# Kernel tuning notes

Hardware: AMD Instinct MI355X
Metric: run time of the kernel (lower is better)

## Reference

```python
import jax, jax.numpy as jnp
import numpy as np
import math

N = 12288
IN_MAIN, IN_MOD = 64, 128
NC_INNER, NC_QK, OUT_MAIN = 16, 8, 64

def setup_inputs() -> dict:
    key = jax.random.key(0)
    ks = jax.random.split(key, 8)
    s = lambda fan_in: 1.0 / np.sqrt(fan_in)
    return {
        "x_main": jax.random.normal(ks[0], (N, IN_MAIN), dtype=jnp.float32),
        "x_mod": jax.random.normal(ks[1], (N, IN_MOD), dtype=jnp.float32),
        "xyz": jax.random.uniform(ks[2], (N, 3), dtype=jnp.float32),
        # MLP E: [in_main+in_mod -> nc_inner -> nc_inner], bias=False (weights stored [in, out])
        "W_e1": jax.random.uniform(ks[3], (IN_MAIN + IN_MOD, NC_INNER), jnp.float32, -s(IN_MAIN + IN_MOD), s(IN_MAIN + IN_MOD)),
        "W_e2": jax.random.uniform(ks[4], (NC_INNER, NC_INNER), jnp.float32, -s(NC_INNER), s(NC_INNER)),
        "W_q": jax.random.uniform(ks[5], (NC_INNER, NC_QK), jnp.float32, -s(NC_INNER), s(NC_INNER)),
        "W_k": jax.random.uniform(ks[6], (NC_INNER, NC_QK), jnp.float32, -s(NC_INNER), s(NC_INNER)),
        "W_v": jax.random.uniform(ks[7], (NC_INNER, OUT_MAIN), jnp.float32, -s(NC_INNER), s(NC_INNER)),
    }

def reference(x_main, x_mod, xyz, W_e1, W_e2, W_q, W_k, W_v):
    # concat 3D + 2D features: [N, in_main+in_mod]
    x = jnp.concatenate((x_main, x_mod), axis=-1)
    # MLP E (bias-free Linear + ReLU per layer): [N, nc_inner]
    h = jax.nn.relu(jax.nn.relu(x @ W_e1) @ W_e2)
    Q = h @ W_q  # [N, nc_qk]
    K = h @ W_k  # [N, nc_qk]
    V = h @ W_v  # [N, out_main]
    scale = 1.0 / math.sqrt(NC_QK)
    scores = (Q @ K.T) * scale          # [N, N] full global attention
    attn = jax.nn.softmax(scores, axis=1)
    return attn @ V                     # [N, out_main]
```

## Files before the change

kernel.cpp:

```cpp
#include <hip/hip_runtime.h>
#include <stdint.h>


#define NN 12288

typedef float    f32x16 __attribute__((ext_vector_type(16)));
typedef short    s16x8  __attribute__((ext_vector_type(8)));
typedef unsigned short u16;

#define MFMA_32x32x16_BF16 __builtin_amdgcn_mfma_f32_32x32x16_bf16

#define OFF_QB   0u
#define OFF_KB   196608u
#define OFF_VT   393216u
#define OFF_PO   2162688u

typedef __attribute__((address_space(3))) void lds_void_t;
typedef const __attribute__((address_space(1))) void gbl_void_t;
__device__ __forceinline__ void gld16(const void* g, void* l) {
    __builtin_amdgcn_global_load_lds((gbl_void_t*)g, (lds_void_t*)l, 16, 0, 0);
}

__device__ __forceinline__ float bf2f(u16 s) {
    union { unsigned int u; float f; } c; c.u = ((unsigned int)s) << 16; return c.f;
}
__device__ __forceinline__ u16 f2bf(float f) {
    union { float f; unsigned int u; } c; c.f = f;
    return (u16)((c.u + 0x8000u) >> 16);
}
__device__ __forceinline__ unsigned int pk2(float a, float b) {
    union { float f; unsigned int u; } ca, cb; ca.f = a; cb.f = b;
    return ((ca.u + 0x8000u) >> 16) | ((cb.u + 0x8000u) & 0xffff0000u);
}
__device__ __forceinline__ f32x16 zf16() {
    f32x16 z;
#pragma unroll
    for (int i = 0; i < 16; ++i) z[i] = 0.f;
    return z;
}
__device__ __forceinline__ s16x8 zs8() {
    s16x8 z;
#pragma unroll
    for (int i = 0; i < 8; ++i) z[i] = 0;
    return z;
}

union U8 { s16x8 v; unsigned int u[4]; };

__global__ __launch_bounds__(256) void k1_qkv(
    const void* __restrict__ xmain, const void* __restrict__ xmod,
    const void* __restrict__ we1, const void* __restrict__ we2,
    const void* __restrict__ wqp, const void* __restrict__ wkp,
    const void* __restrict__ wvp,
    u16* __restrict__ qb, u16* __restrict__ kb, u16* __restrict__ vt)
{
    __shared__ float wf[4608];
    __shared__ int   sflag;
    __shared__ float lh1[64][4][17];
    __shared__ float lh2[64][17];

    const int t = threadIdx.x;
    const int r = t >> 2;
    const int p = t & 3;
    const int row = blockIdx.x * 64 + r;

    if (t == 0) sflag = 0;
    __syncthreads();
    {
        float v = bf2f(((const u16*)xmod)[2 * t]);
        if (fabsf(v) > 16.f) atomicAdd(&sflag, 1);
    }
    __syncthreads();
    const int isf32 = (sflag > 8);

    const float SCL = 0.51006979f;
    if (isf32) {
        const float* a1 = (const float*)we1; const float* a2 = (const float*)we2;
        const float* aq = (const float*)wqp; const float* ak = (const float*)wkp;
        const float* av = (const float*)wvp;
        for (int i = t; i < 4608; i += 256) {
            if      (i < 3072) wf[i] = a1[i];
            else if (i < 3328) wf[i] = a2[i - 3072];
            else if (i < 3456) wf[i] = aq[i - 3328] * SCL;
            else if (i < 3584) wf[i] = ak[i - 3456];
            else               wf[i] = av[i - 3584];
        }
    } else {
        const u16* a1 = (const u16*)we1; const u16* a2 = (const u16*)we2;
        const u16* aq = (const u16*)wqp; const u16* ak = (const u16*)wkp;
        const u16* av = (const u16*)wvp;
        for (int i = t; i < 4608; i += 256) {
            if      (i < 3072) wf[i] = bf2f(a1[i]);
            else if (i < 3328) wf[i] = bf2f(a2[i - 3072]);
            else if (i < 3456) wf[i] = bf2f(aq[i - 3328]) * SCL;
            else if (i < 3584) wf[i] = bf2f(ak[i - 3456]);
            else               wf[i] = bf2f(av[i - 3584]);
        }
    }
    __syncthreads();

    const float* __restrict__ W1 = wf;
    const float* __restrict__ W2 = wf + 3072;
    const float* __restrict__ Wq = wf + 3328;
    const float* __restrict__ Wk = wf + 3456;
    const float* __restrict__ Wv = wf + 3584;

    float h1p[16];
#pragma unroll
    for (int o = 0; o < 16; ++o) h1p[o] = 0.f;

    if (isf32) {
#pragma unroll
        for (int cc = 0; cc < 12; ++cc) {
            const int c = p + cc * 4;
            float4 xv = (c < 16)
                ? ((const float4*)xmain)[(size_t)row * 16 + c]
                : ((const float4*)xmod)[(size_t)row * 32 + (c - 16)];
            float xs[4] = {xv.x, xv.y, xv.z, xv.w};
#pragma unroll
            for (int j = 0; j < 4; ++j) {
                const float* wr = W1 + (c * 4 + j) * 16;
#pragma unroll
                for (int o = 0; o < 16; ++o) h1p[o] += xs[j] * wr[o];
            }
        }
    } else {
#pragma unroll
        for (int cc = 0; cc < 12; ++cc) {
            const int c = p + cc * 4;
            uint2 xv = (c < 16)
                ? ((const uint2*)xmain)[(size_t)row * 16 + c]
                : ((const uint2*)xmod)[(size_t)row * 32 + (c - 16)];
            float xs[4] = { bf2f((u16)(xv.x & 0xffff)), bf2f((u16)(xv.x >> 16)),
                            bf2f((u16)(xv.y & 0xffff)), bf2f((u16)(xv.y >> 16)) };
#pragma unroll
            for (int j = 0; j < 4; ++j) {
                const float* wr = W1 + (c * 4 + j) * 16;
#pragma unroll
                for (int o = 0; o < 16; ++o) h1p[o] += xs[j] * wr[o];
            }
        }
    }
#pragma unroll
    for (int o = 0; o < 16; ++o) lh1[r][p][o] = h1p[o];
    __syncthreads();

    float h1[16];
#pragma unroll
    for (int o = 0; o < 16; ++o)
        h1[o] = fmaxf(lh1[r][0][o] + lh1[r][1][o] + lh1[r][2][o] + lh1[r][3][o], 0.f);

#pragma unroll
    for (int oo = 0; oo < 4; ++oo) {
        const int o = p * 4 + oo;
        float s = 0.f;
#pragma unroll
        for (int j = 0; j < 16; ++j) s += h1[j] * W2[j * 16 + o];
        lh2[r][o] = fmaxf(s, 0.f);
    }
    __syncthreads();

    float h2[16];
#pragma unroll
    for (int j = 0; j < 16; ++j) h2[j] = lh2[r][j];

    {
        float q0 = 0.f, q1 = 0.f, k0 = 0.f, k1 = 0.f;
        const int o = 2 * p;
#pragma unroll
        for (int j = 0; j < 16; ++j) {
            q0 += h2[j] * Wq[j * 8 + o];
            q1 += h2[j] * Wq[j * 8 + o + 1];
            k0 += h2[j] * Wk[j * 8 + o];
            k1 += h2[j] * Wk[j * 8 + o + 1];
        }
        ((unsigned int*)qb)[(size_t)row * 4 + p] = pk2(q0, q1);
        ((unsigned int*)kb)[(size_t)row * 4 + p] = pk2(k0, k1);
    }

    const int tI = row >> 5, kk = row & 31;
#pragma unroll
    for (int c16 = 0; c16 < 16; ++c16) {
        const int c = p * 16 + c16;
        float v = 0.f;
#pragma unroll
        for (int j = 0; j < 16; ++j) v += h2[j] * Wv[j * 64 + c];
        vt[(size_t)tI * 2304 + c * 36 + kk] = f2bf(v);
    }
}

__global__ __launch_bounds__(256, 4) void k2_attn(
    const u16* __restrict__ qb, const u16* __restrict__ kb,
    const u16* __restrict__ vt,
    float* __restrict__ po, float* __restrict__ pl,
    int nsplit, int tiles)
{
    __shared__ union SM {
        uint4 stage[4][2][288];
        struct { float lo[4][64][33]; float ll[4][32]; } ep;
    } sm;

    const int tid  = threadIdx.x;
    const int lane = tid & 63;
    const int half = lane >> 5;
    const int l31  = lane & 31;
    const int w    = tid >> 6;
    const int qt   = blockIdx.x % 384;
    const int sp   = blockIdx.x / 384;
    const int qbase = qt * 32;
    const int key_start = sp * (NN / nsplit) + w * (tiles * 32);
    const int t0 = key_start >> 5;

    const f32x16 Z = zf16();
    s16x8 qf = zs8();
    if (!half) qf = *(const s16x8*)(qb + (size_t)(qbase + l31) * 8);

    f32x16 acc0 = Z, acc1 = Z;
    float ls = 0.f;

    {
        const char* g = (const char*)vt + (size_t)t0 * 4608 + lane * 16;
#pragma unroll
        for (int j = 0; j < 4; ++j)
            gld16(g + j * 1024, &sm.stage[w][0][j * 64]);
        if (lane < 32)
            gld16(g + 4096, &sm.stage[w][0][256]);
    }
    s16x8 ka_c = *(const s16x8*)(kb + (size_t)(key_start + l31) * 8);

    for (int kt = 0; kt < tiles; ++kt) {
        __builtin_amdgcn_s_waitcnt(0x0F70);
        const int cb = kt & 1;
        const bool has_next = (kt + 1 < tiles);

        s16x8 ka_n;
        if (has_next) {
            ka_n = *(const s16x8*)(kb + (size_t)(key_start + (kt + 1) * 32 + l31) * 8);
            const char* g = (const char*)vt + (size_t)(t0 + kt + 1) * 4608 + lane * 16;
#pragma unroll
            for (int j = 0; j < 4; ++j)
                gld16(g + j * 1024, &sm.stage[w][cb ^ 1][j * 64]);
            if (lane < 32)
                gld16(g + 4096, &sm.stage[w][cb ^ 1][256]);
        }

        f32x16 S = MFMA_32x32x16_BF16(ka_c, qf, Z, 0, 0, 0);

        float pr[16];
        float ls0 = 0.f, ls1 = 0.f;
#pragma unroll
        for (int r = 0; r < 8; ++r) {
            pr[r]     = __builtin_amdgcn_exp2f(S[r]);
            pr[r + 8] = __builtin_amdgcn_exp2f(S[r + 8]);
            ls0 += pr[r];
            ls1 += pr[r + 8];
        }
        ls += ls0 + ls1;

        U8 pb0, pb1;
#pragma unroll
        for (int i = 0; i < 4; ++i) {
            pb0.u[i] = pk2(pr[2 * i],     pr[2 * i + 1]);
            pb1.u[i] = pk2(pr[8 + 2 * i], pr[8 + 2 * i + 1]);
        }

        const u16* base = (const u16*)&sm.stage[w][cb][0];
        const u16* r0 = base + l31 * 36 + 4 * half;
        const u16* r1 = base + (32 + l31) * 36 + 4 * half;
        U8 va;
        uint2 x0, x1;
        x0 = *(const uint2*)(r0);       x1 = *(const uint2*)(r0 + 8);
        va.u[0] = x0.x; va.u[1] = x0.y; va.u[2] = x1.x; va.u[3] = x1.y;
        acc0 = MFMA_32x32x16_BF16(va.v, pb0.v, acc0, 0, 0, 0);
        x0 = *(const uint2*)(r1);       x1 = *(const uint2*)(r1 + 8);
        va.u[0] = x0.x; va.u[1] = x0.y; va.u[2] = x1.x; va.u[3] = x1.y;
        acc1 = MFMA_32x32x16_BF16(va.v, pb0.v, acc1, 0, 0, 0);
        x0 = *(const uint2*)(r0 + 16);  x1 = *(const uint2*)(r0 + 24);
        va.u[0] = x0.x; va.u[1] = x0.y; va.u[2] = x1.x; va.u[3] = x1.y;
        acc0 = MFMA_32x32x16_BF16(va.v, pb1.v, acc0, 0, 0, 0);
        x0 = *(const uint2*)(r1 + 16);  x1 = *(const uint2*)(r1 + 24);
        va.u[0] = x0.x; va.u[1] = x0.y; va.u[2] = x1.x; va.u[3] = x1.y;
        acc1 = MFMA_32x32x16_BF16(va.v, pb1.v, acc1, 0, 0, 0);

        if (has_next) ka_c = ka_n;
    }

    __syncthreads();

    ls += __shfl_xor(ls, 32, 64);
    if (lane < 32) sm.ep.ll[w][l31] = ls;
#pragma unroll
    for (int r = 0; r < 16; ++r) {
        const int c = (r & 3) + 8 * (r >> 2) + 4 * half;
        sm.ep.lo[w][c][l31]      = acc0[r];
        sm.ep.lo[w][32 + c][l31] = acc1[r];
    }
    __syncthreads();

    const int rq = tid >> 3;
    const int c0 = (tid & 7) * 8;
    float o[8];
#pragma unroll
    for (int j = 0; j < 8; ++j) {
        o[j] = sm.ep.lo[0][c0 + j][rq] + sm.ep.lo[1][c0 + j][rq] +
               sm.ep.lo[2][c0 + j][rq] + sm.ep.lo[3][c0 + j][rq];
    }
    float4* pov = (float4*)(po + (size_t)sp * (NN * 64) +
                            (size_t)(qbase + rq) * 64 + c0);
    pov[0] = make_float4(o[0], o[1], o[2], o[3]);
    pov[1] = make_float4(o[4], o[5], o[6], o[7]);
    if (tid < 32)
        pl[(size_t)sp * NN + qbase + tid] =
            sm.ep.ll[0][tid] + sm.ep.ll[1][tid] + sm.ep.ll[2][tid] + sm.ep.ll[3][tid];
}

__global__ __launch_bounds__(256) void k3_norm(
    const float4* __restrict__ po, const float* __restrict__ pl,
    float4* __restrict__ out, int nsplit)
{
    const int i = blockIdx.x * 256 + threadIdx.x;
    const int row = i >> 4;
    float l = 0.f;
    float4 o = make_float4(0.f, 0.f, 0.f, 0.f);
    for (int s = 0; s < nsplit; ++s) {
        l += pl[(size_t)s * NN + row];
        float4 p = po[(size_t)s * (NN * 16) + i];
        o.x += p.x; o.y += p.y; o.z += p.z; o.w += p.w;
    }
    const float rl = 1.0f / l;
    out[i] = make_float4(o.x * rl, o.y * rl, o.z * rl, o.w * rl);
}

extern "C" void kernel_launch(void* const* d_in, const int* in_sizes, int n_in,
                              void* d_out, int out_size, void* d_ws, size_t ws_size,
                              hipStream_t stream)
{
    const void* xmain = d_in[0];
    const void* xmod  = d_in[1];
    const void* we1   = d_in[3];
    const void* we2   = d_in[4];
    const void* wq    = d_in[5];
    const void* wk    = d_in[6];
    const void* wv    = d_in[7];

    char* ws = (char*)d_ws;
    u16*   qb   = (u16*)  (ws + OFF_QB);
    u16*   kb   = (u16*)  (ws + OFF_KB);
    u16*   vt   = (u16*)  (ws + OFF_VT);

    int S = 1;
    for (int cand = 8; cand >= 1; cand >>= 1) {
        size_t need = (size_t)OFF_PO + (size_t)cand * (NN * 64 * 4) +
                      (size_t)cand * (NN * 4);
        if (ws_size >= need) { S = cand; break; }
    }
    float* po = (float*)(ws + OFF_PO);
    float* pl = po + (size_t)S * (NN * 64);
    const int tiles = NN / (128 * S);

    k1_qkv<<<192, 256, 0, stream>>>(xmain, xmod, we1, we2, wq, wk, wv,
                                    qb, kb, vt);
    k2_attn<<<384 * S, 256, 0, stream>>>(qb, kb, vt, po, pl, S, tiles);
    k3_norm<<<768, 256, 0, stream>>>((const float4*)po, pl, (float4*)d_out, S);
}
```

Before: 131.2 us.

## Share V tiles across four query waves and store bf16 split partials

The attention kernel is restructured so each block's four waves handle four different 32-row query tiles over the same key range. They cooperatively load one shared double-buffered V tile instead of each wave streaming its own key slice, which cuts LDS use and global V traffic per query and allows higher occupancy (launch bound 4 to 6) and up to 16 key splits. Partial outputs are stored as bf16 instead of fp32 to halve partial-sum traffic, and a hardware packed bf16 conversion builtin is used when available. The cost is a block-wide barrier on every key tile and extra rounding error in the split partials.

New measurement: 131.2 us. About the same (-0.0%).

```diff
diff --git a/kernel.cpp b/kernel.cpp
--- a/kernel.cpp
+++ b/kernel.cpp
@@ -31,6 +31,14 @@
 __device__ __forceinline__ unsigned int pk2(float a, float b) {
     union { float f; unsigned int u; } ca, cb; ca.f = a; cb.f = b;
     return ((ca.u + 0x8000u) >> 16) | ((cb.u + 0x8000u) & 0xffff0000u);
+}
+__device__ __forceinline__ unsigned int pkbf(float a, float b) {
+#if __has_builtin(__builtin_amdgcn_cvt_pk_bf16_f32)
+    auto r = __builtin_amdgcn_cvt_pk_bf16_f32(a, b);
+    union { decltype(r) v; unsigned int u; } c; c.v = r; return c.u;
+#else
+    return pk2(a, b);
+#endif
 }
 __device__ __forceinline__ f32x16 zf16() {
     f32x16 z;
@@ -189,15 +197,15 @@
     }
 }
 
-__global__ __launch_bounds__(256, 4) void k2_attn(
+__global__ __launch_bounds__(256, 6) void k2_attn(
     const u16* __restrict__ qb, const u16* __restrict__ kb,
     const u16* __restrict__ vt,
-    float* __restrict__ po, float* __restrict__ pl,
+    u16* __restrict__ po, float* __restrict__ pl,
     int nsplit, int tiles)
 {
     __shared__ union SM {
-        uint4 stage[4][2][288];
-        struct { float lo[4][64][33]; float ll[4][32]; } ep;
+        uint4 stage[2][288];
+        float sf[2304];
     } sm;
 
     const int tid  = threadIdx.x;
@@ -205,43 +213,41 @@
     const int half = lane >> 5;
     const int l31  = lane & 31;
     const int w    = tid >> 6;
-    const int qt   = blockIdx.x % 384;
-    const int sp   = blockIdx.x / 384;
-    const int qbase = qt * 32;
-    const int key_start = sp * (NN / nsplit) + w * (tiles * 32);
+    const int qB   = (blockIdx.x % 96) * 128;
+    const int sp   = blockIdx.x / 96;
+    const int myq  = qB + 32 * w;
+    const int key_start = sp * (NN / nsplit);
     const int t0 = key_start >> 5;
 
     const f32x16 Z = zf16();
     s16x8 qf = zs8();
-    if (!half) qf = *(const s16x8*)(qb + (size_t)(qbase + l31) * 8);
+    if (!half) qf = *(const s16x8*)(qb + (size_t)(myq + l31) * 8);
 
     f32x16 acc0 = Z, acc1 = Z;
     float ls = 0.f;
 
     {
-        const char* g = (const char*)vt + (size_t)t0 * 4608 + lane * 16;
-#pragma unroll
-        for (int j = 0; j < 4; ++j)
-            gld16(g + j * 1024, &sm.stage[w][0][j * 64]);
-        if (lane < 32)
-            gld16(g + 4096, &sm.stage[w][0][256]);
+        const char* g = (const char*)vt + (size_t)t0 * 4608 + 1152 * w + lane * 16;
+        char* l = (char*)&sm.stage[0][0] + 1152 * w;
+        gld16(g, l);
+        if (lane < 8) gld16(g + 1024, l + 1024);
     }
     s16x8 ka_c = *(const s16x8*)(kb + (size_t)(key_start + l31) * 8);
 
     for (int kt = 0; kt < tiles; ++kt) {
         __builtin_amdgcn_s_waitcnt(0x0F70);
+        __syncthreads();
         const int cb = kt & 1;
         const bool has_next = (kt + 1 < tiles);
 
         s16x8 ka_n;
         if (has_next) {
             ka_n = *(const s16x8*)(kb + (size_t)(key_start + (kt + 1) * 32 + l31) * 8);
-            const char* g = (const char*)vt + (size_t)(t0 + kt + 1) * 4608 + lane * 16;
-#pragma unroll
-            for (int j = 0; j < 4; ++j)
-                gld16(g + j * 1024, &sm.stage[w][cb ^ 1][j * 64]);
-            if (lane < 32)
-                gld16(g + 4096, &sm.stage[w][cb ^ 1][256]);
+            const char* g = (const char*)vt + (size_t)(t0 + kt + 1) * 4608
+                          + 1152 * w + lane * 16;
+            char* l = (char*)&sm.stage[cb ^ 1][0] + 1152 * w;
+            gld16(g, l);
+            if (lane < 8) gld16(g + 1024, l + 1024);
         }
 
         f32x16 S = MFMA_32x32x16_BF16(ka_c, qf, Z, 0, 0, 0);
@@ -260,11 +266,11 @@
         U8 pb0, pb1;
 #pragma unroll
         for (int i = 0; i < 4; ++i) {
-            pb0.u[i] = pk2(pr[2 * i],     pr[2 * i + 1]);
-            pb1.u[i] = pk2(pr[8 + 2 * i], pr[8 + 2 * i + 1]);
-        }
-
-        const u16* base = (const u16*)&sm.stage[w][cb][0];
+            pb0.u[i] = pkbf(pr[2 * i],     pr[2 * i + 1]);
+            pb1.u[i] = pkbf(pr[8 + 2 * i], pr[8 + 2 * i + 1]);
+        }
+
+        const u16* base = (const u16*)&sm.stage[cb][0];
         const u16* r0 = base + l31 * 36 + 4 * half;
         const u16* r1 = base + (32 + l31) * 36 + 4 * half;
         U8 va;
@@ -285,50 +291,52 @@
         if (has_next) ka_c = ka_n;
     }
 
-    __syncthreads();
-
     ls += __shfl_xor(ls, 32, 64);
-    if (lane < 32) sm.ep.ll[w][l31] = ls;
-#pragma unroll
-    for (int r = 0; r < 16; ++r) {
-        const int c = (r & 3) + 8 * (r >> 2) + 4 * half;
-        sm.ep.lo[w][c][l31]      = acc0[r];
-        sm.ep.lo[w][32 + c][l31] = acc1[r];
-    }
-    __syncthreads();
-
-    const int rq = tid >> 3;
-    const int c0 = (tid & 7) * 8;
-    float o[8];
-#pragma unroll
-    for (int j = 0; j < 8; ++j) {
-        o[j] = sm.ep.lo[0][c0 + j][rq] + sm.ep.lo[1][c0 + j][rq] +
-               sm.ep.lo[2][c0 + j][rq] + sm.ep.lo[3][c0 + j][rq];
-    }
-    float4* pov = (float4*)(po + (size_t)sp * (NN * 64) +
-                            (size_t)(qbase + rq) * 64 + c0);
-    pov[0] = make_float4(o[0], o[1], o[2], o[3]);
-    pov[1] = make_float4(o[4], o[5], o[6], o[7]);
-    if (tid < 32)
-        pl[(size_t)sp * NN + qbase + tid] =
-            sm.ep.ll[0][tid] + sm.ep.ll[1][tid] + sm.ep.ll[2][tid] + sm.ep.ll[3][tid];
+
+    u16* poS = po + (size_t)sp * (NN * 64);
+    for (int j = 0; j < 4; ++j) {
+        __syncthreads();
+        if (w == j) {
+#pragma unroll
+            for (int r = 0; r < 16; ++r) {
+                const int c = (r & 3) + 8 * (r >> 2) + 4 * half;
+                sm.sf[c * 33 + l31]        = acc0[r];
+                sm.sf[(32 + c) * 33 + l31] = acc1[r];
+            }
+            if (lane < 32) sm.sf[2112 + l31] = ls;
+        }
+        __syncthreads();
+        const int rq = tid >> 3;
+        const int c0 = (tid & 7) * 8;
+        unsigned int u0 = pkbf(sm.sf[(c0 + 0) * 33 + rq], sm.sf[(c0 + 1) * 33 + rq]);
+        unsigned int u1 = pkbf(sm.sf[(c0 + 2) * 33 + rq], sm.sf[(c0 + 3) * 33 + rq]);
+        unsigned int u2 = pkbf(sm.sf[(c0 + 4) * 33 + rq], sm.sf[(c0 + 5) * 33 + rq]);
+        unsigned int u3 = pkbf(sm.sf[(c0 + 6) * 33 + rq], sm.sf[(c0 + 7) * 33 + rq]);
+        *(uint4*)(poS + (size_t)(qB + 32 * j + rq) * 64 + c0) =
+            make_uint4(u0, u1, u2, u3);
+        if (tid < 32)
+            pl[(size_t)sp * NN + qB + 32 * j + tid] = sm.sf[2112 + tid];
+    }
 }
 
 __global__ __launch_bounds__(256) void k3_norm(
-    const float4* __restrict__ po, const float* __restrict__ pl,
+    const u16* __restrict__ po, const float* __restrict__ pl,
     float4* __restrict__ out, int nsplit)
 {
     const int i = blockIdx.x * 256 + threadIdx.x;
     const int row = i >> 4;
+    const int c0 = (i & 15) * 4;
     float l = 0.f;
-    float4 o = make_float4(0.f, 0.f, 0.f, 0.f);
+    float o0 = 0.f, o1 = 0.f, o2 = 0.f, o3 = 0.f;
     for (int s = 0; s < nsplit; ++s) {
         l += pl[(size_t)s * NN + row];
-        float4 p = po[(size_t)s * (NN * 16) + i];
-        o.x += p.x; o.y += p.y; o.z += p.z; o.w += p.w;
+        uint2 p = *(const uint2*)(po + (size_t)s * (NN * 64) +
+                                  (size_t)row * 64 + c0);
+        o0 += bf2f((u16)(p.x & 0xffff)); o1 += bf2f((u16)(p.x >> 16));
+        o2 += bf2f((u16)(p.y & 0xffff)); o3 += bf2f((u16)(p.y >> 16));
     }
     const float rl = 1.0f / l;
-    out[i] = make_float4(o.x * rl, o.y * rl, o.z * rl, o.w * rl);
+    out[i] = make_float4(o0 * rl, o1 * rl, o2 * rl, o3 * rl);
 }
 
 extern "C" void kernel_launch(void* const* d_in, const int* in_sizes, int n_in,
@@ -349,17 +357,17 @@
     u16*   vt   = (u16*)  (ws + OFF_VT);
 
     int S = 1;
-    for (int cand = 8; cand >= 1; cand >>= 1) {
-        size_t need = (size_t)OFF_PO + (size_t)cand * (NN * 64 * 4) +
+    for (int cand = 16; cand >= 1; cand >>= 1) {
+        size_t need = (size_t)OFF_PO + (size_t)cand * (NN * 64 * 2) +
                       (size_t)cand * (NN * 4);
         if (ws_size >= need) { S = cand; break; }
     }
-    float* po = (float*)(ws + OFF_PO);
-    float* pl = po + (size_t)S * (NN * 64);
-    const int tiles = NN / (128 * S);
+    u16*   po = (u16*)(ws + OFF_PO);
+    float* pl = (float*)(ws + OFF_PO + (size_t)S * (NN * 64 * 2));
+    const int tiles = NN / (32 * S);
 
     k1_qkv<<<192, 256, 0, stream>>>(xmain, xmod, we1, we2, wq, wk, wv,
                                     qb, kb, vt);
-    k2_attn<<<384 * S, 256, 0, stream>>>(qb, kb, vt, po, pl, S, tiles);
-    k3_norm<<<768, 256, 0, stream>>>((const float4*)po, pl, (float4*)d_out, S);
-}
+    k2_attn<<<96 * S, 256, 0, stream>>>(qb, kb, vt, po, pl, S, tiles);
+    k3_norm<<<768, 256, 0, stream>>>(po, pl, (float4*)d_out, S);
+}
```
